# Kernel tuning notes

Hardware: AMD Instinct MI355X
Metric: run time of the kernel (lower is better)

## Reference

```python
import jax, jax.numpy as jnp
import numpy as np

N = 10000
E = 320000
D = 256
EPS = 1e-5

def layer_norm(x, g, b):
    mu = jnp.mean(x, axis=-1, keepdims=True)
    var = jnp.mean(jnp.square(x - mu), axis=-1, keepdims=True)
    return (x - mu) * jax.lax.rsqrt(var + EPS) * g + b

def linear(x, w, b):
    # w: [in, out]
    return x @ w + b

def setup_inputs() -> dict:
    key = jax.random.key(0)
    ks = jax.random.split(key, 20)
    s = 1.0 / np.sqrt(D)
    inp = {
        'x': jax.random.normal(ks[0], (N, D), jnp.float32),
        'edge_index': jax.random.randint(ks[1], (2, E), 0, N, jnp.int64),
        'edge_weight': jax.random.normal(ks[2], (E,), jnp.float32),
        'wq': jax.random.normal(ks[3], (D, D), jnp.float32) * s,
        'bq': jnp.zeros((D,), jnp.float32),
        'wk': jax.random.normal(ks[4], (D, D), jnp.float32) * s,
        'bk': jnp.zeros((D,), jnp.float32),
        'wv': jax.random.normal(ks[5], (D, D), jnp.float32) * s,
        'bv': jnp.zeros((D,), jnp.float32),
        'ws': jax.random.normal(ks[6], (D, D), jnp.float32) * s,
        'bs': jnp.zeros((D,), jnp.float32),
        'we': jax.random.normal(ks[7], (1, 1), jnp.float32),
        'be': jnp.zeros((1,), jnp.float32),
        'g1': jnp.ones((D,), jnp.float32),
        'b1': jnp.zeros((D,), jnp.float32),
        'g2': jnp.ones((D,), jnp.float32),
        'b2': jnp.zeros((D,), jnp.float32),
        'w_ff1': jax.random.normal(ks[8], (D, 2 * D), jnp.float32) * s,
        'b_ff1': jnp.zeros((2 * D,), jnp.float32),
        'w_ff2': jax.random.normal(ks[9], (2 * D, D), jnp.float32) * (1.0 / np.sqrt(2 * D)),
        'b_ff2': jnp.zeros((D,), jnp.float32),
    }
    return inp

def reference(x, edge_index, edge_weight, wq, bq, wk, bk, wv, bv, ws, bs, we, be,
              g1, b1, g2, b2, w_ff1, b_ff1, w_ff2, b_ff2):
    n = x.shape[0]
    scale = x.shape[-1] ** (-0.5)
    q = linear(x, wq, bq)
    k = linear(x, wk, bk)
    v = linear(x, wv, bv)
    src, dst = edge_index[0], edge_index[1]
    # per-edge attention scores: dot(q[dst], k[src]) * scale
    scores = jnp.sum(q[dst] * k[src], axis=-1) * scale
    scores = scores + (edge_weight[:, None] @ we + be)[:, 0]
    # two-pass segment softmax over dst
    seg_max = jax.ops.segment_max(scores, dst, num_segments=n)
    exp_s = jnp.exp(scores - seg_max[dst])
    denom = jax.ops.segment_sum(exp_s, dst, num_segments=n)
    attn = exp_s / jnp.maximum(denom[dst], 1e-12)
    # scatter-add weighted messages
    message = v[src] * attn[:, None]  # [E, D]
    out = jax.ops.segment_sum(message, dst, num_segments=n)
    x = layer_norm(x + out + linear(x, ws, bs), g1, b1)
    ffn = linear(jax.nn.gelu(linear(x, w_ff1, b_ff1)), w_ff2, b_ff2)
    x = layer_norm(x + ffn, g2, b2)
    return x
```

## Files before the change

### kernel.cpp

```cpp
#include <hip/hip_runtime.h>
#include <math.h>

#define N_NODES 10000
#define N_EDGES 320000
#define DIM 256
#define BCAP 128

typedef __attribute__((ext_vector_type(8))) short bf16x8;
typedef __attribute__((ext_vector_type(4))) float fx4;

typedef __attribute__((address_space(3))) unsigned lds_u32;
typedef __attribute__((address_space(1))) const unsigned gbl_u32;


__device__ __forceinline__ float gelu_tanh(float x) {
  const float k0 = 0.7978845608028654f;
  float x3 = x * x * x;
  return 0.5f * x * (1.0f + tanhf(k0 * (x + 0.044715f * x3)));
}

__device__ __forceinline__ unsigned short f2bf(float f) {
  unsigned u = __float_as_uint(f);
  unsigned r = 0x7FFFu + ((u >> 16) & 1u);
  return (unsigned short)((u + r) >> 16);
}

__device__ __forceinline__ float bf_lo(unsigned u) { return __uint_as_float(u << 16); }
__device__ __forceinline__ float bf_hi(unsigned u) { return __uint_as_float(u & 0xFFFF0000u); }


#define SEG_QKVS 262144
#define SEG_FF1 131072
#define SEG_FF2 131072
#define SEG_BIAS 1024
#define SEG_CONV 320000
#define SEG_ZCNT 10000
#define PREP_TOTAL (SEG_QKVS + SEG_FF1 + SEG_FF2 + SEG_BIAS + SEG_CONV + SEG_ZCNT)

__global__ __launch_bounds__(256) void prep_all_kernel(
    const float* __restrict__ wq, const float* __restrict__ wk,
    const float* __restrict__ wv, const float* __restrict__ ws,
    const float* __restrict__ bq, const float* __restrict__ bk,
    const float* __restrict__ bv, const float* __restrict__ bs,
    const float* __restrict__ wff1, const float* __restrict__ wff2,
    const float* __restrict__ x,
    unsigned short* __restrict__ wt_qkvs, float* __restrict__ bias_qkvs,
    unsigned short* __restrict__ wt_ff1, unsigned short* __restrict__ wt_ff2,
    unsigned short* __restrict__ xb, unsigned* __restrict__ cnt) {
  int id = blockIdx.x * 256 + threadIdx.x;
  if (id < SEG_QKVS) {
    const int n = id >> 8, k = id & 255;
    const float* w = (n < 256) ? wq : (n < 512) ? wk : (n < 768) ? wv : ws;
    wt_qkvs[id] = f2bf(w[k * 256 + (n & 255)]);
    return;
  }
  id -= SEG_QKVS;
  if (id < SEG_FF1) {
    const int n = id >> 8, k = id & 255;
    wt_ff1[id] = f2bf(wff1[k * 512 + n]);
    return;
  }
  id -= SEG_FF1;
  if (id < SEG_FF2) {
    const int n = id >> 9, k = id & 511;
    wt_ff2[id] = f2bf(wff2[k * 256 + n]);
    return;
  }
  id -= SEG_FF2;
  if (id < SEG_BIAS) {
    bias_qkvs[id] = (id < 256) ? bq[id] : (id < 512) ? bk[id & 255]
                    : (id < 768) ? bv[id & 255] : bs[id & 255];
    return;
  }
  id -= SEG_BIAS;
  if (id < SEG_CONV) {
    const int base = id * 8;
    float4 a = *(const float4*)(x + base);
    float4 b = *(const float4*)(x + base + 4);
    unsigned short h[8] = {f2bf(a.x), f2bf(a.y), f2bf(a.z), f2bf(a.w),
                           f2bf(b.x), f2bf(b.y), f2bf(b.z), f2bf(b.w)};
    *(uint4*)(xb + base) = *(const uint4*)h;
    return;
  }
  id -= SEG_CONV;
  if (id < SEG_ZCNT) cnt[id] = 0u;
}

template <int GELU, int WF32, int WB16, int SPLIT>
__global__ __launch_bounds__(256) void mfma_gemm(
    const unsigned short* __restrict__ A, int lda,
    const unsigned short* __restrict__ Bt,
    const float* __restrict__ bias,
    const float* __restrict__ xres,
    float* __restrict__ C, int ldc,
    unsigned short* __restrict__ Cb, int ldcb,
    int M, int K,
    const int* __restrict__ ei, const float* __restrict__ ew,
    const float* __restrict__ we, const float* __restrict__ be,
    unsigned* __restrict__ cnt, uint2* __restrict__ es_csr) {
  __shared__ char lds[32768];
  const int tid = threadIdx.x;

  if (SPLIT) {
    const int bid = blockIdx.y * gridDim.x + blockIdx.x;
    const int stride = gridDim.x * gridDim.y * 256;
    const float wes = we[0], bes = be[0];
    for (int e = bid * 256 + tid; e < N_EDGES; e += stride) {
      const int dst = ei[N_EDGES + e];
      const unsigned pos = atomicAdd(cnt + dst, 1u);
      uint2 es;
      es.x = (unsigned)ei[e];
      es.y = __float_as_uint(ew[e] * wes + bes);
      es_csr[(size_t)dst * BCAP + pos] = es;
    }
  }

  const int l = tid & 63;
  const int wid = tid >> 6;
  const int wrow = (wid & 1) * 32;
  const int wcol = (wid >> 1) * 32;
  const int bm = blockIdx.y * 64;
  const int bn = blockIdx.x * 64;

  fx4 acc[2][2];
#pragma unroll
  for (int i = 0; i < 2; i++)
#pragma unroll
    for (int j = 0; j < 2; j++) acc[i][j] = (fx4)(0.0f);

#define STAGE(BUFOFF, KB)                                                      \
  {                                                                            \
    _Pragma("unroll") for (int i = 0; i < 2; i++) {                            \
      const int id = i * 256 + tid;                                            \
      const int row = id >> 3;                                                 \
      const int ccs = (id & 7) ^ (row & 7);                                    \
      __builtin_amdgcn_global_load_lds(                                        \
          (gbl_u32*)(A + (size_t)(bm + row) * lda + (KB) + ccs * 8),           \
          (lds_u32*)(lds + (BUFOFF) + id * 16), 16, 0, 0);                     \
    }                                                                          \
    _Pragma("unroll") for (int i = 0; i < 2; i++) {                            \
      const int id = i * 256 + tid;                                            \
      const int row = id >> 3;                                                 \
      const int ccs = (id & 7) ^ (row & 7);                                    \
      __builtin_amdgcn_global_load_lds(                                        \
          (gbl_u32*)(Bt + (size_t)(bn + row) * K + (KB) + ccs * 8),            \
          (lds_u32*)(lds + (BUFOFF) + 8192 + id * 16), 16, 0, 0);              \
    }                                                                          \
  }

  STAGE(0, 0);

  unsigned cur = 0;
  for (int kb = 0; kb < K; kb += 64) {
    if (kb + 64 < K) {
      STAGE((cur ^ 1) * 16384, kb + 64);
      asm volatile("s_waitcnt vmcnt(4)" ::: "memory");
    } else {
      asm volatile("s_waitcnt vmcnt(0)" ::: "memory");
    }
    __builtin_amdgcn_s_barrier();
    __builtin_amdgcn_sched_barrier(0);

    const char* As = lds + cur * 16384;
    const char* Bs = As + 8192;
#pragma unroll
    for (int kk = 0; kk < 2; kk++) {
      const int kbyte = (kk * 64 + ((l >> 4) << 4)) ^ ((l & 7) << 4);
      bf16x8 af[2], bg[2];
#pragma unroll
      for (int f = 0; f < 2; f++) {
        const int ar = wrow + f * 16 + (l & 15);
        af[f] = *(const bf16x8*)(As + ar * 128 + kbyte);
        const int br = wcol + f * 16 + (l & 15);
        bg[f] = *(const bf16x8*)(Bs + br * 128 + kbyte);
      }
#pragma unroll
      for (int fr = 0; fr < 2; fr++)
#pragma unroll
        for (int fc = 0; fc < 2; fc++)
          acc[fr][fc] = __builtin_amdgcn_mfma_f32_16x16x32_bf16(
              af[fr], bg[fc], acc[fr][fc], 0, 0, 0);
    }
    __builtin_amdgcn_s_barrier();
    cur ^= 1;
  }
#undef STAGE

#pragma unroll
  for (int fr = 0; fr < 2; fr++) {
    const int m0 = bm + wrow + fr * 16 + ((l >> 4) << 2);
#pragma unroll
    for (int fc = 0; fc < 2; fc++) {
      const int n = bn + wcol + fc * 16 + (l & 15);
      const float bn_ = bias[n];
      fx4 v = acc[fr][fc];
#pragma unroll
      for (int r = 0; r < 4; r++) {
        const int row = m0 + r;
        if (row < M) {
          float o = v[r] + bn_;
          if (GELU) o = gelu_tanh(o);
          if (SPLIT) {
            const int seg = n >> 8, nn = n & 255;
            if (seg == 3)
              C[(size_t)row * 256 + nn] = o + xres[(size_t)row * 256 + nn];
            else
              Cb[(size_t)seg * (N_NODES * DIM) + (size_t)row * 256 + nn] = f2bf(o);
          } else {
            if (WF32) C[(size_t)row * ldc + n] = o;
            if (WB16) Cb[(size_t)row * ldcb + n] = f2bf(o);
          }
        }
      }
    }
  }
}

__global__ __launch_bounds__(64) void agg_fused_kernel(
    const unsigned* __restrict__ cnt, const uint2* __restrict__ es_csr,
    const unsigned short* __restrict__ qb,
    const unsigned short* __restrict__ kb, const unsigned short* __restrict__ vb,
    const float* __restrict__ sbuf,
    const float* __restrict__ g, const float* __restrict__ b,
    float* __restrict__ out, unsigned short* __restrict__ outb) {
  const int node = blockIdx.x;
  const int lane = threadIdx.x;
  const int grp = lane >> 4;
  const int t = lane & 15;
  const int start = node * BCAP;
  const int deg = min((int)cnt[node], BCAP);
  const int end = start + deg;

  const uint4 qA = *(const uint4*)(qb + (size_t)node * 256 + t * 16);
  const uint4 qB = *(const uint4*)(qb + (size_t)node * 256 + t * 16 + 8);
  float qf[16];
  qf[0] = bf_lo(qA.x);  qf[1] = bf_hi(qA.x);
  qf[2] = bf_lo(qA.y);  qf[3] = bf_hi(qA.y);
  qf[4] = bf_lo(qA.z);  qf[5] = bf_hi(qA.z);
  qf[6] = bf_lo(qA.w);  qf[7] = bf_hi(qA.w);
  qf[8] = bf_lo(qB.x);  qf[9] = bf_hi(qB.x);
  qf[10] = bf_lo(qB.y); qf[11] = bf_hi(qB.y);
  qf[12] = bf_lo(qB.z); qf[13] = bf_hi(qB.z);
  qf[14] = bf_lo(qB.w); qf[15] = bf_hi(qB.w);

  float m = -3.4e38f, dsum = 0.f;
  float a0 = 0.f, a1 = 0.f, a2 = 0.f, a3 = 0.f;

  int ea = start + grp * 2;
  int eb_ = ea + 1;
  bool va = ea < end, vbd = eb_ < end;
  int sa = 0, sb = 0;
  float ba = 0.f, bb = 0.f;
  if (va) { const uint2 es = es_csr[ea]; sa = (int)es.x; ba = __uint_as_float(es.y); }
  if (vbd) { const uint2 es = es_csr[eb_]; sb = (int)es.x; bb = __uint_as_float(es.y); }
  uint4 kAa = *(const uint4*)(kb + (size_t)sa * 256 + t * 16);
  uint4 kBa = *(const uint4*)(kb + (size_t)sa * 256 + t * 16 + 8);
  uint4 kAb = *(const uint4*)(kb + (size_t)sb * 256 + t * 16);
  uint4 kBb = *(const uint4*)(kb + (size_t)sb * 256 + t * 16 + 8);

  for (int base = start; base < end; base += 8) {
    const int s0 = __shfl(sa, 0), s1 = __shfl(sa, 16);
    const int s2 = __shfl(sa, 32), s3 = __shfl(sa, 48);
    const int s4 = __shfl(sb, 0), s5 = __shfl(sb, 16);
    const int s6 = __shfl(sb, 32), s7 = __shfl(sb, 48);
    const uint2 v0 = *(const uint2*)(vb + (size_t)s0 * 256 + lane * 4);
    const uint2 v1 = *(const uint2*)(vb + (size_t)s1 * 256 + lane * 4);
    const uint2 v2 = *(const uint2*)(vb + (size_t)s2 * 256 + lane * 4);
    const uint2 v3 = *(const uint2*)(vb + (size_t)s3 * 256 + lane * 4);
    const uint2 v4 = *(const uint2*)(vb + (size_t)s4 * 256 + lane * 4);
    const uint2 v5 = *(const uint2*)(vb + (size_t)s5 * 256 + lane * 4);
    const uint2 v6 = *(const uint2*)(vb + (size_t)s6 * 256 + lane * 4);
    const uint2 v7 = *(const uint2*)(vb + (size_t)s7 * 256 + lane * 4);

    const int na = base + 8 + grp * 2;
    const int nb = na + 1;
    const bool va_n = na < end, vb_n = nb < end;
    int sa_n = 0, sb_n = 0;
    float ba_n = 0.f, bb_n = 0.f;
    if (va_n) { const uint2 es = es_csr[na]; sa_n = (int)es.x; ba_n = __uint_as_float(es.y); }
    if (vb_n) { const uint2 es = es_csr[nb]; sb_n = (int)es.x; bb_n = __uint_as_float(es.y); }

    float da = qf[0] * bf_lo(kAa.x);
    float db = qf[0] * bf_lo(kAb.x);
    da = fmaf(qf[1], bf_hi(kAa.x), da);  db = fmaf(qf[1], bf_hi(kAb.x), db);
    da = fmaf(qf[2], bf_lo(kAa.y), da);  db = fmaf(qf[2], bf_lo(kAb.y), db);
    da = fmaf(qf[3], bf_hi(kAa.y), da);  db = fmaf(qf[3], bf_hi(kAb.y), db);
    da = fmaf(qf[4], bf_lo(kAa.z), da);  db = fmaf(qf[4], bf_lo(kAb.z), db);
    da = fmaf(qf[5], bf_hi(kAa.z), da);  db = fmaf(qf[5], bf_hi(kAb.z), db);
    da = fmaf(qf[6], bf_lo(kAa.w), da);  db = fmaf(qf[6], bf_lo(kAb.w), db);
    da = fmaf(qf[7], bf_hi(kAa.w), da);  db = fmaf(qf[7], bf_hi(kAb.w), db);
    da = fmaf(qf[8], bf_lo(kBa.x), da);  db = fmaf(qf[8], bf_lo(kBb.x), db);
    da = fmaf(qf[9], bf_hi(kBa.x), da);  db = fmaf(qf[9], bf_hi(kBb.x), db);
    da = fmaf(qf[10], bf_lo(kBa.y), da); db = fmaf(qf[10], bf_lo(kBb.y), db);
    da = fmaf(qf[11], bf_hi(kBa.y), da); db = fmaf(qf[11], bf_hi(kBb.y), db);
    da = fmaf(qf[12], bf_lo(kBa.z), da); db = fmaf(qf[12], bf_lo(kBb.z), db);
    da = fmaf(qf[13], bf_hi(kBa.z), da); db = fmaf(qf[13], bf_hi(kBb.z), db);
    da = fmaf(qf[14], bf_lo(kBa.w), da); db = fmaf(qf[14], bf_lo(kBb.w), db);
    da = fmaf(qf[15], bf_hi(kBa.w), da); db = fmaf(qf[15], bf_hi(kBb.w), db);
    da += __shfl_xor(da, 1);  db += __shfl_xor(db, 1);
    da += __shfl_xor(da, 2);  db += __shfl_xor(db, 2);
    da += __shfl_xor(da, 4);  db += __shfl_xor(db, 4);
    da += __shfl_xor(da, 8);  db += __shfl_xor(db, 8);
    const float sca = va ? fmaf(da, 0.0625f, ba) : -3.4e38f;
    const float scb = vbd ? fmaf(db, 0.0625f, bb) : -3.4e38f;

    const uint4 kAa_n = *(const uint4*)(kb + (size_t)sa_n * 256 + t * 16);
    const uint4 kBa_n = *(const uint4*)(kb + (size_t)sa_n * 256 + t * 16 + 8);
    const uint4 kAb_n = *(const uint4*)(kb + (size_t)sb_n * 256 + t * 16);
    const uint4 kBb_n = *(const uint4*)(kb + (size_t)sb_n * 256 + t * 16 + 8);

    const float c0 = __shfl(sca, 0), c1 = __shfl(sca, 16);
    const float c2 = __shfl(sca, 32), c3 = __shfl(sca, 48);
    const float c4 = __shfl(scb, 0), c5 = __shfl(scb, 16);
    const float c6 = __shfl(scb, 32), c7 = __shfl(scb, 48);

    const float mx = fmaxf(fmaxf(fmaxf(c0, c1), fmaxf(c2, c3)),
                           fmaxf(fmaxf(c4, c5), fmaxf(c6, c7)));
    const float mn = fmaxf(m, mx);
    const float scale = __expf(m - mn);
    const float w0 = __expf(c0 - mn), w1 = __expf(c1 - mn);
    const float w2 = __expf(c2 - mn), w3 = __expf(c3 - mn);
    const float w4 = __expf(c4 - mn), w5 = __expf(c5 - mn);
    const float w6 = __expf(c6 - mn), w7 = __expf(c7 - mn);
    dsum = fmaf(dsum, scale, ((w0 + w1) + (w2 + w3)) + ((w4 + w5) + (w6 + w7)));

    float t0 = a0 * scale;
    t0 = fmaf(w0, bf_lo(v0.x), t0); t0 = fmaf(w1, bf_lo(v1.x), t0);
    t0 = fmaf(w2, bf_lo(v2.x), t0); t0 = fmaf(w3, bf_lo(v3.x), t0);
    t0 = fmaf(w4, bf_lo(v4.x), t0); t0 = fmaf(w5, bf_lo(v5.x), t0);
    t0 = fmaf(w6, bf_lo(v6.x), t0); t0 = fmaf(w7, bf_lo(v7.x), t0);
    a0 = t0;
    float t1 = a1 * scale;
    t1 = fmaf(w0, bf_hi(v0.x), t1); t1 = fmaf(w1, bf_hi(v1.x), t1);
    t1 = fmaf(w2, bf_hi(v2.x), t1); t1 = fmaf(w3, bf_hi(v3.x), t1);
    t1 = fmaf(w4, bf_hi(v4.x), t1); t1 = fmaf(w5, bf_hi(v5.x), t1);
    t1 = fmaf(w6, bf_hi(v6.x), t1); t1 = fmaf(w7, bf_hi(v7.x), t1);
    a1 = t1;
    float t2 = a2 * scale;
    t2 = fmaf(w0, bf_lo(v0.y), t2); t2 = fmaf(w1, bf_lo(v1.y), t2);
    t2 = fmaf(w2, bf_lo(v2.y), t2); t2 = fmaf(w3, bf_lo(v3.y), t2);
    t2 = fmaf(w4, bf_lo(v4.y), t2); t2 = fmaf(w5, bf_lo(v5.y), t2);
    t2 = fmaf(w6, bf_lo(v6.y), t2); t2 = fmaf(w7, bf_lo(v7.y), t2);
    a2 = t2;
    float t3 = a3 * scale;
    t3 = fmaf(w0, bf_hi(v0.y), t3); t3 = fmaf(w1, bf_hi(v1.y), t3);
    t3 = fmaf(w2, bf_hi(v2.y), t3); t3 = fmaf(w3, bf_hi(v3.y), t3);
    t3 = fmaf(w4, bf_hi(v4.y), t3); t3 = fmaf(w5, bf_hi(v5.y), t3);
    t3 = fmaf(w6, bf_hi(v6.y), t3); t3 = fmaf(w7, bf_hi(v7.y), t3);
    a3 = t3;
    m = mn;

    sa = sa_n; sb = sb_n;
    ba = ba_n; bb = bb_n;
    va = va_n; vbd = vb_n;
    kAa = kAa_n; kBa = kBa_n;
    kAb = kAb_n; kBb = kBb_n;
  }
  const float inv = 1.0f / fmaxf(dsum, 1e-12f);

  const float4 sv = *(const float4*)(sbuf + (size_t)node * 256 + lane * 4);
  float r0 = a0 * inv + sv.x;
  float r1 = a1 * inv + sv.y;
  float r2 = a2 * inv + sv.z;
  float r3 = a3 * inv + sv.w;

  float sum = r0 + r1 + r2 + r3;
#pragma unroll
  for (int off = 32; off > 0; off >>= 1) sum += __shfl_xor(sum, off);
  const float mu = sum * (1.0f / 256.0f);
  const float d0 = r0 - mu, d1 = r1 - mu, d2 = r2 - mu, d3 = r3 - mu;
  float vs = d0 * d0 + d1 * d1 + d2 * d2 + d3 * d3;
#pragma unroll
  for (int off = 32; off > 0; off >>= 1) vs += __shfl_xor(vs, off);
  const float rs = rsqrtf(vs * (1.0f / 256.0f) + 1e-5f);

  const float4 gv = *(const float4*)(g + lane * 4);
  const float4 bv = *(const float4*)(b + lane * 4);
  float4 o;
  o.x = d0 * rs * gv.x + bv.x;
  o.y = d1 * rs * gv.y + bv.y;
  o.z = d2 * rs * gv.z + bv.z;
  o.w = d3 * rs * gv.w + bv.w;
  *(float4*)(out + (size_t)node * 256 + lane * 4) = o;
  uint2 pk;
  pk.x = (unsigned)f2bf(o.x) | ((unsigned)f2bf(o.y) << 16);
  pk.y = (unsigned)f2bf(o.z) | ((unsigned)f2bf(o.w) << 16);
  *(uint2*)(outb + (size_t)node * 256 + lane * 4) = pk;
}


__global__ __launch_bounds__(256) void ln2_kernel(
    const float* __restrict__ x1, const float* __restrict__ y,
    const float* __restrict__ g, const float* __restrict__ b,
    float* __restrict__ out) {
  __shared__ float red[4];
  const int row = blockIdx.x;
  const int t = threadIdx.x;
  float v = x1[(size_t)row * 256 + t] + y[(size_t)row * 256 + t];
  float s = v;
#pragma unroll
  for (int off = 32; off > 0; off >>= 1) s += __shfl_xor(s, off);
  if ((t & 63) == 0) red[t >> 6] = s;
  __syncthreads();
  float tot = red[0] + red[1] + red[2] + red[3];
  __syncthreads();
  const float mu = tot * (1.0f / 256.0f);
  const float d = v - mu;
  float vs = d * d;
#pragma unroll
  for (int off = 32; off > 0; off >>= 1) vs += __shfl_xor(vs, off);
  if ((t & 63) == 0) red[t >> 6] = vs;
  __syncthreads();
  float vtot = red[0] + red[1] + red[2] + red[3];
  const float r = rsqrtf(vtot * (1.0f / 256.0f) + 1e-5f);
  out[(size_t)row * 256 + t] = d * r * g[t] + b[t];
}


extern "C" void kernel_launch(void* const* d_in, const int* in_sizes, int n_in,
                              void* d_out, int out_size, void* d_ws,
                              size_t ws_size, hipStream_t stream) {
  const float* x = (const float*)d_in[0];
  const int* ei = (const int*)d_in[1];
  const float* ew = (const float*)d_in[2];
  const float* wq = (const float*)d_in[3];
  const float* bq = (const float*)d_in[4];
  const float* wk = (const float*)d_in[5];
  const float* bk = (const float*)d_in[6];
  const float* wv = (const float*)d_in[7];
  const float* bv = (const float*)d_in[8];
  const float* wsm = (const float*)d_in[9];
  const float* bs = (const float*)d_in[10];
  const float* we = (const float*)d_in[11];
  const float* be = (const float*)d_in[12];
  const float* g1 = (const float*)d_in[13];
  const float* b1 = (const float*)d_in[14];
  const float* g2 = (const float*)d_in[15];
  const float* b2 = (const float*)d_in[16];
  const float* wff1 = (const float*)d_in[17];
  const float* bff1 = (const float*)d_in[18];
  const float* wff2 = (const float*)d_in[19];
  const float* bff2 = (const float*)d_in[20];
  float* out = (float*)d_out;

  unsigned short* qb = (unsigned short*)d_ws;
  unsigned short* kbp = qb + 2560000;
  unsigned short* vbp = qb + 5120000;
  float* sbuf = (float*)(qb + 7680000);
  uint2* es_csr = (uint2*)(sbuf + 2560000);
  unsigned* cnt = (unsigned*)(es_csr + (size_t)N_NODES * BCAP);
  float* x1 = (float*)(cnt + N_NODES);
  float* y = x1 + 2560000;
  unsigned short* x1b = (unsigned short*)(y + 2560000);
  unsigned short* h_b = x1b + 2560000;
  unsigned short* xb = h_b;
  unsigned short* wt_qkvs = h_b + 5120000;
  unsigned short* wt_ff1 = wt_qkvs + 262144;
  unsigned short* wt_ff2 = wt_ff1 + 131072;
  float* bias_qkvs = (float*)(wt_ff2 + 131072);

  dim3 blk(256);
  const int mb = (N_NODES + 63) / 64;

  prep_all_kernel<<<(PREP_TOTAL + 255) / 256, blk, 0, stream>>>(
      wq, wk, wv, wsm, bq, bk, bv, bs, wff1, wff2, x,
      wt_qkvs, bias_qkvs, wt_ff1, wt_ff2, xb, cnt);

  mfma_gemm<0, 0, 0, 1><<<dim3(16, mb), blk, 0, stream>>>(
      xb, 256, wt_qkvs, bias_qkvs, x, sbuf, 0, qb, 0, N_NODES, 256,
      ei, ew, we, be, cnt, es_csr);

  agg_fused_kernel<<<N_NODES, dim3(64), 0, stream>>>(
      cnt, es_csr, qb, kbp, vbp, sbuf, g1, b1, x1, x1b);

  mfma_gemm<1, 0, 1, 0><<<dim3(8, mb), blk, 0, stream>>>(
      x1b, 256, wt_ff1, bff1, nullptr, (float*)nullptr, 0, h_b, 512, N_NODES, 256,
      nullptr, nullptr, nullptr, nullptr, nullptr, nullptr);

  mfma_gemm<0, 1, 0, 0><<<dim3(4, mb), blk, 0, stream>>>(
      h_b, 512, wt_ff2, bff2, nullptr, y, 256, (unsigned short*)nullptr, 0, N_NODES, 512,
      nullptr, nullptr, nullptr, nullptr, nullptr, nullptr);

  ln2_kernel<<<N_NODES, blk, 0, stream>>>(x1, y, g2, b2, out);
}
```

Baseline: 138.5 us.

## Replace global-atomic edge bucketing with two-pass partitioned scatter

Edge-to-destination bucketing moves out of the QKV GEMM prologue into two dedicated kernels. The first bins edges into 250 partitions of 40 nodes using LDS atomics plus one global atomic per partition per block. The second builds per-node CSR slots with LDS atomics. This removes 320k global atomics on random addresses and uncoalesced writes, at the cost of two extra launches, an intermediate buffer with fixed capacity (PCAP 2048 per partition), and packing src/dst into 16 bits each.

```diff
diff --git a/kernel.cpp b/kernel.cpp
--- a/kernel.cpp
+++ b/kernel.cpp
@@ -5,6 +5,11 @@
 #define N_EDGES 320000
 #define DIM 256
 #define BCAP 128
+
+#define P_PARTS 250
+#define NPP 40
+#define PCAP 2048
+#define EPT 16
 
 typedef __attribute__((ext_vector_type(8))) short bf16x8;
 typedef __attribute__((ext_vector_type(4))) float fx4;
@@ -34,7 +39,7 @@
 #define SEG_FF2 131072
 #define SEG_BIAS 1024
 #define SEG_CONV 320000
-#define SEG_ZCNT 10000
+#define SEG_ZCNT 256
 #define PREP_TOTAL (SEG_QKVS + SEG_FF1 + SEG_FF2 + SEG_BIAS + SEG_CONV + SEG_ZCNT)
 
 __global__ __launch_bounds__(256) void prep_all_kernel(
@@ -46,7 +51,7 @@
     const float* __restrict__ x,
     unsigned short* __restrict__ wt_qkvs, float* __restrict__ bias_qkvs,
     unsigned short* __restrict__ wt_ff1, unsigned short* __restrict__ wt_ff2,
-    unsigned short* __restrict__ xb, unsigned* __restrict__ cnt) {
+    unsigned short* __restrict__ xb, unsigned* __restrict__ pcnt) {
   int id = blockIdx.x * 256 + threadIdx.x;
   if (id < SEG_QKVS) {
     const int n = id >> 8, k = id & 255;
@@ -83,7 +88,84 @@
     return;
   }
   id -= SEG_CONV;
-  if (id < SEG_ZCNT) cnt[id] = 0u;
+  if (id < SEG_ZCNT) pcnt[id] = 0u;
+}
+
+__global__ __launch_bounds__(512) void scatter_p1(
+    const int* __restrict__ ei, const float* __restrict__ ew,
+    const float* __restrict__ we, const float* __restrict__ be,
+    unsigned* __restrict__ pcnt, uint2* __restrict__ pbuf) {
+  __shared__ unsigned lcnt[P_PARTS];
+  __shared__ unsigned lbase[P_PARTS];
+  const int tid = threadIdx.x;
+  for (int i = tid; i < P_PARTS; i += 512) lcnt[i] = 0;
+  __syncthreads();
+  const float wes = we[0], bes = be[0];
+  const int e0 = blockIdx.x * (512 * EPT);
+
+  unsigned pp[EPT];
+  unsigned rr[EPT];
+  unsigned sv[EPT];
+  float ebv[EPT];
+#pragma unroll
+  for (int j = 0; j < EPT; j++) {
+    const int e = e0 + j * 512 + tid;
+    pp[j] = 0;
+    rr[j] = 0xFFFFFFFFu;
+    if (e < N_EDGES) {
+      const int dst = ei[N_EDGES + e];
+      const int src = ei[e];
+      const int p = dst / NPP;
+      sv[j] = (unsigned)dst | ((unsigned)src << 16);
+      ebv[j] = fmaf(ew[e], wes, bes);
+      pp[j] = (unsigned)p;
+      rr[j] = atomicAdd(&lcnt[p], 1u);
+    }
+  }
+  __syncthreads();
+  for (int i = tid; i < P_PARTS; i += 512) {
+    const unsigned c = lcnt[i];
+    lbase[i] = c ? atomicAdd(&pcnt[i], c) : 0u;
+  }
+  __syncthreads();
+#pragma unroll
+  for (int j = 0; j < EPT; j++) {
+    if (rr[j] != 0xFFFFFFFFu) {
+      const unsigned pos = lbase[pp[j]] + rr[j];
+      if (pos < PCAP) {
+        uint2 rec;
+        rec.x = sv[j];
+        rec.y = __float_as_uint(ebv[j]);
+        pbuf[(size_t)pp[j] * PCAP + pos] = rec;
+      }
+    }
+  }
+}
+
+__global__ __launch_bounds__(256) void scatter_p2(
+    const unsigned* __restrict__ pcnt, const uint2* __restrict__ pbuf,
+    unsigned* __restrict__ cnt, uint2* __restrict__ es_csr) {
+  __shared__ unsigned lcnt[NPP];
+  const int p = blockIdx.x;
+  const int tid = threadIdx.x;
+  if (tid < NPP) lcnt[tid] = 0;
+  __syncthreads();
+  const int n0 = p * NPP;
+  const int tot = min((int)pcnt[p], PCAP);
+  for (int i = tid; i < tot; i += 256) {
+    const uint2 rec = pbuf[(size_t)p * PCAP + i];
+    const int dst = (int)(rec.x & 0xFFFFu);
+    const int src = (int)(rec.x >> 16);
+    const unsigned r = atomicAdd(&lcnt[dst - n0], 1u);
+    if (r < BCAP) {
+      uint2 o;
+      o.x = (unsigned)src;
+      o.y = rec.y;
+      es_csr[(size_t)dst * BCAP + r] = o;
+    }
+  }
+  __syncthreads();
+  if (tid < NPP) cnt[n0 + tid] = lcnt[tid];
 }
 
 template <int GELU, int WF32, int WB16, int SPLIT>
@@ -94,26 +176,9 @@
     const float* __restrict__ xres,
     float* __restrict__ C, int ldc,
     unsigned short* __restrict__ Cb, int ldcb,
-    int M, int K,
-    const int* __restrict__ ei, const float* __restrict__ ew,
-    const float* __restrict__ we, const float* __restrict__ be,
-    unsigned* __restrict__ cnt, uint2* __restrict__ es_csr) {
+    int M, int K) {
   __shared__ char lds[32768];
   const int tid = threadIdx.x;
-
-  if (SPLIT) {
-    const int bid = blockIdx.y * gridDim.x + blockIdx.x;
-    const int stride = gridDim.x * gridDim.y * 256;
-    const float wes = we[0], bes = be[0];
-    for (int e = bid * 256 + tid; e < N_EDGES; e += stride) {
-      const int dst = ei[N_EDGES + e];
-      const unsigned pos = atomicAdd(cnt + dst, 1u);
-      uint2 es;
-      es.x = (unsigned)ei[e];
-      es.y = __float_as_uint(ew[e] * wes + bes);
-      es_csr[(size_t)dst * BCAP + pos] = es;
-    }
-  }
 
   const int l = tid & 63;
   const int wid = tid >> 6;
@@ -458,28 +523,31 @@
   unsigned short* wt_ff1 = wt_qkvs + 262144;
   unsigned short* wt_ff2 = wt_ff1 + 131072;
   float* bias_qkvs = (float*)(wt_ff2 + 131072);
+  unsigned* pcnt = (unsigned*)(bias_qkvs + 1024);
+  uint2* pbuf = (uint2*)(pcnt + 256);
 
   dim3 blk(256);
   const int mb = (N_NODES + 63) / 64;
 
   prep_all_kernel<<<(PREP_TOTAL + 255) / 256, blk, 0, stream>>>(
       wq, wk, wv, wsm, bq, bk, bv, bs, wff1, wff2, x,
-      wt_qkvs, bias_qkvs, wt_ff1, wt_ff2, xb, cnt);
+      wt_qkvs, bias_qkvs, wt_ff1, wt_ff2, xb, pcnt);
+
+  scatter_p1<<<(N_EDGES + 512 * EPT - 1) / (512 * EPT), dim3(512), 0, stream>>>(
+      ei, ew, we, be, pcnt, pbuf);
+  scatter_p2<<<P_PARTS, blk, 0, stream>>>(pcnt, pbuf, cnt, es_csr);
 
   mfma_gemm<0, 0, 0, 1><<<dim3(16, mb), blk, 0, stream>>>(
-      xb, 256, wt_qkvs, bias_qkvs, x, sbuf, 0, qb, 0, N_NODES, 256,
-      ei, ew, we, be, cnt, es_csr);
+      xb, 256, wt_qkvs, bias_qkvs, x, sbuf, 0, qb, 0, N_NODES, 256);
 
   agg_fused_kernel<<<N_NODES, dim3(64), 0, stream>>>(
       cnt, es_csr, qb, kbp, vbp, sbuf, g1, b1, x1, x1b);
 
   mfma_gemm<1, 0, 1, 0><<<dim3(8, mb), blk, 0, stream>>>(
-      x1b, 256, wt_ff1, bff1, nullptr, (float*)nullptr, 0, h_b, 512, N_NODES, 256,
-      nullptr, nullptr, nullptr, nullptr, nullptr, nullptr);
+      x1b, 256, wt_ff1, bff1, nullptr, (float*)nullptr, 0, h_b, 512, N_NODES, 256);
 
   mfma_gemm<0, 1, 0, 0><<<dim3(4, mb), blk, 0, stream>>>(
-      h_b, 512, wt_ff2, bff2, nullptr, y, 256, (unsigned short*)nullptr, 0, N_NODES, 512,
-      nullptr, nullptr, nullptr, nullptr, nullptr, nullptr);
+      h_b, 512, wt_ff2, bff2, nullptr, y, 256, (unsigned short*)nullptr, 0, N_NODES, 512);
 
   ln2_kernel<<<N_NODES, blk, 0, stream>>>(x1, y, g2, b2, out);
 }
```

Result: no change. 139.2 us (+0.5%).
